# Kernel tuning notes

Hardware: AMD Instinct MI355X
Metric: run time of the kernel (lower is better)

## Reference

```python
import jax, jax.numpy as jnp
import numpy as np

HID = 128
NLAYERS = 8
LAT = 32
DIM_IN = 63 + 15 + LAT  # pe(xyz,L=10)=3+60, pe(shift,L=2)=3+12, latent=32 -> 110


def _pe(x, L):
    # NeRF positional encoding, include_input=True, freq-major [sin3,cos3] per freq
    freqs = (2.0 ** jnp.arange(L)).astype(x.dtype)
    xf = x[..., None, :] * freqs[:, None]                      # [..., L, 3]
    sc = jnp.concatenate([jnp.sin(xf), jnp.cos(xf)], axis=-1)  # [..., L, 6]
    return jnp.concatenate([x, sc.reshape(*x.shape[:-1], 6 * L)], axis=-1)


def setup_inputs() -> dict:
    key = jax.random.key(0)
    ks = jax.random.split(key, 24)
    B, P, V = 2, 32768, 5023
    d = {}
    d["pts"] = jax.random.normal(ks[0], (B, P, 3), jnp.float32)
    d["deformed_mesh_pts"] = jax.random.normal(ks[1], (B, V, 3), jnp.float32)
    d["cano_verts"] = jax.random.normal(ks[2], (1, V, 3), jnp.float32)
    d["motion_latent"] = jax.random.normal(ks[3], (B, P, LAT), jnp.float32)
    for i in range(NLAYERS):
        fin = DIM_IN if i == 0 else (DIM_IN + HID if i == NLAYERS // 2 else HID)
        d[f"w{i}"] = jax.random.normal(ks[4 + i], (HID, fin), jnp.float32) / np.sqrt(fin).astype(np.float32)
        d[f"b{i}"] = jnp.zeros((HID,), jnp.float32)
    d["w_out"] = jax.random.normal(ks[20], (3, HID), jnp.float32) * 0.01
    d["b_out"] = jnp.zeros((3,), jnp.float32)
    return d


def reference(pts, deformed_mesh_pts, cano_verts, motion_latent,
              w0, b0, w1, b1, w2, b2, w3, b3, w4, b4, w5, b5, w6, b6, w7, b7,
              w_out, b_out):
    # mesh-guided shift per vertex
    mesh_shift = cano_verts - deformed_mesh_pts                 # [B,V,3]
    # point-to-point NN search (squared euclidean cdist + argmin)
    d2 = ((pts ** 2).sum(-1)[:, :, None]
          + (deformed_mesh_pts ** 2).sum(-1)[:, None, :]
          - 2.0 * jnp.einsum('bpc,bvc->bpv', pts, deformed_mesh_pts))  # [B,P,V]
    d2 = jnp.maximum(d2, 0.0)
    idx = jnp.argmin(d2, axis=-1)                               # [B,P]
    dist = jnp.min(d2, axis=-1)                                 # [B,P]
    weight = jnp.exp(-dist)[..., None]                          # 1/exp(dist)
    gidx = jnp.broadcast_to(idx[:, :, None], idx.shape + (3,))
    gshift = jnp.take_along_axis(mesh_shift, gidx, axis=1) * weight  # [B,P,3]
    # deformation MLP with skip connection at layer 4
    initial = jnp.concatenate([_pe(pts, 10), _pe(gshift, 2), motion_latent], axis=-1)
    ws = [w0, w1, w2, w3, w4, w5, w6, w7]
    bs = [b0, b1, b2, b3, b4, b5, b6, b7]
    x = initial
    last_feat = x
    for i in range(NLAYERS):
        inp = jnp.concatenate([initial, x], axis=-1) if i == NLAYERS // 2 else x
        x = inp @ ws[i].T + bs[i]
        last_feat = x  # pre-activation feature (out_feat_ls[-1])
        x = jax.nn.relu(x)
    mlp_shift = x @ w_out.T + b_out                             # [B,P,3]
    pts_shifts = gshift + mlp_shift
    return pts + pts_shifts, last_feat
```

## Files before the change

kernel.cpp:

```cpp
#include <hip/hip_runtime.h>
#include <math.h>

typedef unsigned short ushort_t;
typedef unsigned int   uint_t;
typedef __attribute__((ext_vector_type(8)))  short bf16x8;
typedef __attribute__((ext_vector_type(16))) float f32x16;

#define NPTS   65536
#define NV     5023
#define LATD   32
#define KF     110
#define FSTR   112

__device__ __forceinline__ ushort_t f2bf(float f) {
  union { float f; unsigned u; } x; x.f = f;
  unsigned r = x.u + 0x7fffu + ((x.u >> 16) & 1u);
  return (ushort_t)(r >> 16);
}
__device__ __forceinline__ float bf2f(ushort_t u) {
  union { unsigned u; float f; } x; x.u = ((unsigned)u) << 16;
  return x.f;
}
__device__ __forceinline__ uint_t packsplit(float v) {
  const ushort_t h = f2bf(v);
  const ushort_t l = f2bf(v - bf2f(h));
  return (uint_t)h | ((uint_t)l << 16);
}


__global__ __launch_bounds__(256, 4) void k_nnfeat(
    const float* __restrict__ pts, const float* __restrict__ dm,
    const float* __restrict__ cano, const float* __restrict__ lat,
    const float* __restrict__ w0, const float* __restrict__ w1,
    const float* __restrict__ w2, const float* __restrict__ w3,
    const float* __restrict__ w4, const float* __restrict__ w5,
    const float* __restrict__ w6, const float* __restrict__ w7,
    uint_t* __restrict__ feat, float* __restrict__ base3,
    ushort_t* __restrict__ wsWh, ushort_t* __restrict__ wsWl)
{
  const int tid = threadIdx.x;

  if (tid < 144) {
    const int e = blockIdx.x * 144 + tid;
    const int p = e >> 14, local = e & 16383;
    const int j   = local & 7;
    const int lh  = (local >> 3) & 1;
    const int l31 = (local >> 4) & 31;
    const int tn  = (local >> 9) & 3;
    const int ks  = (local >> 11) & 7;
    const int n = tn*32 + l31;
    const int k = ks*16 + lh*8 + j;
    float v;
    if (p == 0)      v = (k < KF) ? w0[n*110 + k] : 0.f;
    else if (p == 1) v = w1[n*128 + k];
    else if (p == 2) v = w2[n*128 + k];
    else if (p == 3) v = w3[n*128 + k];
    else if (p == 4) v = (k < KF) ? w4[n*238 + k] : 0.f;
    else if (p == 5) v = w4[n*238 + KF + k];
    else if (p == 6) v = w5[n*128 + k];
    else if (p == 7) v = w6[n*128 + k];
    else             v = w7[n*128 + k];
    const ushort_t h = f2bf(v);
    wsWh[e] = h;
    wsWl[e] = f2bf(v - bf2f(h));
  }

  __shared__ float4 sV[512];
  __shared__ float  sD[64];
  __shared__ int    sI[64];

  const int lane = tid & 63, w = tid >> 6;
  const int slot = lane >> 4, s = lane & 15;
  const int g0 = blockIdx.x * 64;
  const int b  = blockIdx.x >> 9;
  const float* __restrict__ dmb = dm + b * NV * 3;
  const int pbase = g0 + w*16 + slot*4;

  float px[4], py[4], pz[4], p2[4], bs[4]; int bi[4];
  #pragma unroll
  for (int j = 0; j < 4; ++j) {
    px[j] = pts[(pbase+j)*3+0]; py[j] = pts[(pbase+j)*3+1]; pz[j] = pts[(pbase+j)*3+2];
    p2[j] = fmaf(px[j],px[j], fmaf(py[j],py[j], pz[j]*pz[j]));
    bs[j] = 3.4e38f; bi[j] = 0;
  }

  for (int v0 = 0; v0 < NV; v0 += 512) {
    __syncthreads();
    #pragma unroll
    for (int it = 0; it < 2; ++it) {
      const int i = it*256 + tid;
      const int v = v0 + i;
      float4 t;
      if (v < NV) {
        const float x = dmb[v*3+0], y = dmb[v*3+1], z = dmb[v*3+2];
        t = make_float4(x, y, z, fmaf(x,x, fmaf(y,y, z*z)));
      } else {
        t = make_float4(0.f, 0.f, 0.f, __builtin_inff());
      }
      sV[i] = t;
    }
    __syncthreads();
    #pragma unroll 8
    for (int k = 0; k < 32; ++k) {
      const float4 t = sV[k*16 + s];
      const int vi = v0 + k*16 + s;
      #pragma unroll
      for (int j = 0; j < 4; ++j) {
        const float dot = fmaf(px[j], t.x, fmaf(py[j], t.y, pz[j]*t.z));
        float d2 = fmaf(-2.f, dot, p2[j] + t.w);
        d2 = fmaxf(d2, 0.f);
        if (d2 < bs[j]) { bs[j] = d2; bi[j] = vi; }
      }
    }
  }

  #pragma unroll
  for (int off = 1; off <= 8; off <<= 1) {
    #pragma unroll
    for (int j = 0; j < 4; ++j) {
      const float ob = __shfl_xor(bs[j], off, 64);
      const int   oi = __shfl_xor(bi[j], off, 64);
      const bool take = (ob < bs[j]) || ((ob == bs[j]) && (oi < bi[j]));
      if (take) { bs[j] = ob; bi[j] = oi; }
    }
  }
  if (s == 0) {
    #pragma unroll
    for (int j = 0; j < 4; ++j) {
      sD[w*16 + slot*4 + j] = bs[j];
      sI[w*16 + slot*4 + j] = bi[j];
    }
  }
  __syncthreads();

  const int p = tid & 63, slice = tid >> 6;
  const int g = g0 + p;
  const float wd = sD[p];
  const int   wi = sI[p];

  const float qx = pts[g*3+0], qy = pts[g*3+1], qz = pts[g*3+2];
  const float wgt = expf(-wd);
  const float sx = (cano[wi*3+0] - dmb[wi*3+0]) * wgt;
  const float sy = (cano[wi*3+1] - dmb[wi*3+1]) * wgt;
  const float sz = (cano[wi*3+2] - dmb[wi*3+2]) * wgt;

  uint_t* __restrict__ fr = feat + (size_t)g * FSTR;

  if (slice == 0) {
    base3[g*3+0] = qx + sx; base3[g*3+1] = qy + sy; base3[g*3+2] = qz + sz;
    fr[0] = packsplit(qx); fr[1] = packsplit(qy); fr[2] = packsplit(qz);
    #pragma unroll
    for (int f = 0; f < 3; ++f) {
      const float F = (float)(1 << f);
      float s0,c0,s1,c1,s2,c2;
      sincosf(qx*F,&s0,&c0); sincosf(qy*F,&s1,&c1); sincosf(qz*F,&s2,&c2);
      const int k = 3 + 6*f;
      fr[k+0]=packsplit(s0); fr[k+1]=packsplit(s1); fr[k+2]=packsplit(s2);
      fr[k+3]=packsplit(c0); fr[k+4]=packsplit(c1); fr[k+5]=packsplit(c2);
    }
    fr[110] = 0; fr[111] = 0;
  } else if (slice == 1) {
    #pragma unroll
    for (int f = 3; f < 7; ++f) {
      const float F = (float)(1 << f);
      float s0,c0,s1,c1,s2,c2;
      sincosf(qx*F,&s0,&c0); sincosf(qy*F,&s1,&c1); sincosf(qz*F,&s2,&c2);
      const int k = 3 + 6*f;
      fr[k+0]=packsplit(s0); fr[k+1]=packsplit(s1); fr[k+2]=packsplit(s2);
      fr[k+3]=packsplit(c0); fr[k+4]=packsplit(c1); fr[k+5]=packsplit(c2);
    }
  } else if (slice == 2) {
    #pragma unroll
    for (int f = 7; f < 10; ++f) {
      const float F = (float)(1 << f);
      float s0,c0,s1,c1,s2,c2;
      sincosf(qx*F,&s0,&c0); sincosf(qy*F,&s1,&c1); sincosf(qz*F,&s2,&c2);
      const int k = 3 + 6*f;
      fr[k+0]=packsplit(s0); fr[k+1]=packsplit(s1); fr[k+2]=packsplit(s2);
      fr[k+3]=packsplit(c0); fr[k+4]=packsplit(c1); fr[k+5]=packsplit(c2);
    }
    #pragma unroll
    for (int j = 0; j < 16; ++j) fr[78+j] = packsplit(lat[g*LATD + j]);
  } else {
    fr[63]=packsplit(sx); fr[64]=packsplit(sy); fr[65]=packsplit(sz);
    #pragma unroll
    for (int f = 0; f < 2; ++f) {
      const float F = (float)(1 << f);
      float s0,c0,s1,c1,s2,c2;
      sincosf(sx*F,&s0,&c0); sincosf(sy*F,&s1,&c1); sincosf(sz*F,&s2,&c2);
      const int k = 66 + 6*f;
      fr[k+0]=packsplit(s0); fr[k+1]=packsplit(s1); fr[k+2]=packsplit(s2);
      fr[k+3]=packsplit(c0); fr[k+4]=packsplit(c1); fr[k+5]=packsplit(c2);
    }
    #pragma unroll
    for (int j = 16; j < 32; ++j) fr[78+j] = packsplit(lat[g*LATD + j]);
  }
}


union U4 { uint_t u[4]; bf16x8 v; };

__device__ __forceinline__ void zero4(f32x16 (&a)[4]) {
  #pragma unroll
  for (int i = 0; i < 4; ++i) a[i] = (f32x16)(0.f);
}

__device__ __forceinline__ void load_feat_frags(
    const uint_t* __restrict__ fr, bf16x8 (&Xh)[8], bf16x8 (&Xl)[8], int lh)
{
  #pragma unroll
  for (int ks = 0; ks < 7; ++ks) {
    const int k0 = ks*16 + lh*8;
    const uint4 ua = *(const uint4*)(fr + k0);
    const uint4 ub = *(const uint4*)(fr + k0 + 4);
    U4 H, L;
    H.u[0] = (ua.x & 0xffffu) | (ua.y << 16);
    H.u[1] = (ua.z & 0xffffu) | (ua.w << 16);
    H.u[2] = (ub.x & 0xffffu) | (ub.y << 16);
    H.u[3] = (ub.z & 0xffffu) | (ub.w << 16);
    L.u[0] = (ua.x >> 16) | (ua.y & 0xffff0000u);
    L.u[1] = (ua.z >> 16) | (ua.w & 0xffff0000u);
    L.u[2] = (ub.x >> 16) | (ub.y & 0xffff0000u);
    L.u[3] = (ub.z >> 16) | (ub.w & 0xffff0000u);
    Xh[ks] = H.v; Xl[ks] = L.v;
  }
}

__device__ __forceinline__ void load_slab(bf16x8 (&wh)[4], bf16x8 (&wl)[4],
    const ushort_t* __restrict__ Wh, const ushort_t* __restrict__ Wl,
    int ks, int l31, int lh)
{
  const int lo = l31*16 + lh*8;
  #pragma unroll
  for (int tn = 0; tn < 4; ++tn) {
    const int off = (ks*4 + tn)*512 + lo;
    wh[tn] = *(const bf16x8*)(Wh + off);
    wl[tn] = *(const bf16x8*)(Wl + off);
  }
}

__device__ __forceinline__ void mfma_slab(f32x16 (&acc)[4],
    const bf16x8 (&wh)[4], const bf16x8 (&wl)[4],
    const bf16x8& xh, const bf16x8& xl)
{
  #pragma unroll
  for (int tn = 0; tn < 4; ++tn) {
    acc[tn] = __builtin_amdgcn_mfma_f32_32x32x16_bf16(wh[tn], xh, acc[tn], 0,0,0);
    acc[tn] = __builtin_amdgcn_mfma_f32_32x32x16_bf16(wl[tn], xh, acc[tn], 0,0,0);
    acc[tn] = __builtin_amdgcn_mfma_f32_32x32x16_bf16(wh[tn], xl, acc[tn], 0,0,0);
  }
}

template<int NKS, bool TAIL>
__device__ __forceinline__ void run_panel(f32x16 (&acc)[4],
    const ushort_t* __restrict__ Wh, const ushort_t* __restrict__ Wl,
    const ushort_t* __restrict__ WhN, const ushort_t* __restrict__ WlN,
    bf16x8 (&wbh)[2][4], bf16x8 (&wbl)[2][4],
    const bf16x8 (&Xh)[8], const bf16x8 (&Xl)[8], int l31, int lh)
{
  #pragma unroll
  for (int ks = 0; ks < NKS; ++ks) {
    const int b = ks & 1;
    mfma_slab(acc, wbh[b], wbl[b], Xh[ks], Xl[ks]);
    if (ks + 2 < NKS) {
      load_slab(wbh[b], wbl[b], Wh, Wl, ks + 2, l31, lh);
    } else if (TAIL) {
      load_slab(wbh[b], wbl[b], WhN, WlN, ks & 1, l31, lh);
    }
  }
}

__device__ __forceinline__ void bias_relu(f32x16 (&acc)[4],
    const float* __restrict__ bias, int lh)
{
  #pragma unroll
  for (int tn = 0; tn < 4; ++tn)
    #pragma unroll
    for (int b = 0; b < 4; ++b) {
      const float4 b4 = *(const float4*)(bias + tn*32 + 8*b + 4*lh);
      acc[tn][4*b+0] = fmaxf(acc[tn][4*b+0] + b4.x, 0.f);
      acc[tn][4*b+1] = fmaxf(acc[tn][4*b+1] + b4.y, 0.f);
      acc[tn][4*b+2] = fmaxf(acc[tn][4*b+2] + b4.z, 0.f);
      acc[tn][4*b+3] = fmaxf(acc[tn][4*b+3] + b4.w, 0.f);
// ... 119 lines not shown
  build_frags(acc, Xh, Xl, lh);

  zero4(acc);
  run_panel<8,false>(acc, wsWh + 8*16384, wsWl + 8*16384,
                          (const ushort_t*)0, (const ushort_t*)0, wbh, wbl, Xh, Xl, l31, lh);

  float* __restrict__ sFw = &sF[wid][0];
  #pragma unroll
  for (int tn = 0; tn < 4; ++tn)
    #pragma unroll
    for (int b = 0; b < 4; ++b) {
      const int n0 = tn*32 + 8*b + 4*lh;
      const float4 bv = *(const float4*)(sB + 7*128 + n0);
      const float v0 = acc[tn][4*b+0] + bv.x;
      const float v1 = acc[tn][4*b+1] + bv.y;
      const float v2 = acc[tn][4*b+2] + bv.z;
      const float v3 = acc[tn][4*b+3] + bv.w;
      *(float4*)(sFw + l31*132 + n0) = make_float4(v0, v1, v2, v3);
      acc[tn][4*b+0] = fmaxf(v0, 0.f);
      acc[tn][4*b+1] = fmaxf(v1, 0.f);
      acc[tn][4*b+2] = fmaxf(v2, 0.f);
      acc[tn][4*b+3] = fmaxf(v3, 0.f);
    }

  asm volatile("s_waitcnt lgkmcnt(0)" ::: "memory");
  __builtin_amdgcn_sched_barrier(0);

  float* __restrict__ out1 = out + (size_t)NPTS * 3;
  #pragma unroll
  for (int i = 0; i < 16; ++i) {
    const int idx = i*64 + lane;
    const int p = idx >> 5, q = idx & 31;
    const float4 v = *(const float4*)(sFw + p*132 + q*4);
    *(float4*)(out1 + (size_t)(p0 + p)*128 + q*4) = v;
  }

  float dotc[3];
  #pragma unroll
  for (int c = 0; c < 3; ++c) {
    float a = 0.f;
    #pragma unroll
    for (int tn = 0; tn < 4; ++tn)
      #pragma unroll
      for (int b = 0; b < 4; ++b) {
        const int n0 = tn*32 + 8*b + 4*lh;
        const float4 w4 = *(const float4*)(sB + 1024 + c*128 + n0);
        a = fmaf(acc[tn][4*b+0], w4.x, a);
        a = fmaf(acc[tn][4*b+1], w4.y, a);
        a = fmaf(acc[tn][4*b+2], w4.z, a);
        a = fmaf(acc[tn][4*b+3], w4.w, a);
      }
    a += __shfl_xor(a, 32, 64);
    dotc[c] = a;
  }
  if (lh == 0) {
    const int g = p0 + l31;
    #pragma unroll
    for (int c = 0; c < 3; ++c)
      out[g*3 + c] = base3[g*3 + c] + dotc[c] + sB[1408 + c];
  }
}

extern "C" void kernel_launch(void* const* d_in, const int* in_sizes, int n_in,
                              void* d_out, int out_size, void* d_ws, size_t ws_size,
                              hipStream_t stream)
{
  const float* pts  = (const float*)d_in[0];
  const float* dm   = (const float*)d_in[1];
  const float* cano = (const float*)d_in[2];
  const float* lat  = (const float*)d_in[3];
  const float* w[8]; const float* b[8];
  for (int i = 0; i < 8; ++i) {
    w[i] = (const float*)d_in[4 + 2*i];
    b[i] = (const float*)d_in[5 + 2*i];
  }
  const float* w_out = (const float*)d_in[20];
  const float* b_out = (const float*)d_in[21];
  float* out = (float*)d_out;

  uint_t*   feat  = (uint_t*)d_ws;
  float*    base3 = (float*)((char*)d_ws + (size_t)NPTS*FSTR*4);
  ushort_t* wsWh  = (ushort_t*)((char*)base3 + (size_t)NPTS*3*4);
  ushort_t* wsWl  = wsWh + 147456;

  k_nnfeat<<<1024, 256, 0, stream>>>(pts, dm, cano, lat,
      w[0],w[1],w[2],w[3],w[4],w[5],w[6],w[7], feat, base3, wsWh, wsWl);
  k_mlp<<<NPTS/128, 256, 0, stream>>>(feat, base3, wsWh, wsWl,
      b[0],b[1],b[2],b[3],b[4],b[5],b[6],b[7], w_out, b_out, out);
}
```

Measured before the change: 252.2 us.

## Split NN search into packed-FMA group minima pass with exact rescan of candidate groups

Adds a prep kernel that converts the weights to bf16 hi/lo and precomputes vertex pairs as (-2x,-2y,-2z,|v|^2) in pair-interleaved form. The NN kernel then gives each wave a quarter of the vertices and one point per lane. A first pass computes per-group minima with two-wide packed FMAs; a second pass rescans, with the original exact distance formula, only the groups whose minimum is within a small margin of the global minimum. This removes the per-vertex compare/select and LDS staging from most of the search, but adds an extra launch, a vpre buffer and reliance on the fixed margin for correct argmin.

```diff
diff --git a/kernel.cpp b/kernel.cpp
--- a/kernel.cpp
+++ b/kernel.cpp
@@ -5,12 +5,15 @@
 typedef unsigned int   uint_t;
 typedef __attribute__((ext_vector_type(8)))  short bf16x8;
 typedef __attribute__((ext_vector_type(16))) float f32x16;
+typedef __attribute__((ext_vector_type(2)))  float f32x2;
 
 #define NPTS   65536
 #define NV     5023
 #define LATD   32
 #define KF     110
 #define FSTR   112
+#define NPAIR  2512
+#define QPAIR  628
 
 __device__ __forceinline__ ushort_t f2bf(float f) {
   union { float f; unsigned u; } x; x.f = f;
@@ -27,21 +30,17 @@
   return (uint_t)h | ((uint_t)l << 16);
 }
 
-
-__global__ __launch_bounds__(256, 4) void k_nnfeat(
-    const float* __restrict__ pts, const float* __restrict__ dm,
-    const float* __restrict__ cano, const float* __restrict__ lat,
+__global__ __launch_bounds__(256) void k_prep(
+    const float* __restrict__ dm,
     const float* __restrict__ w0, const float* __restrict__ w1,
     const float* __restrict__ w2, const float* __restrict__ w3,
     const float* __restrict__ w4, const float* __restrict__ w5,
     const float* __restrict__ w6, const float* __restrict__ w7,
-    uint_t* __restrict__ feat, float* __restrict__ base3,
-    ushort_t* __restrict__ wsWh, ushort_t* __restrict__ wsWl)
-{
-  const int tid = threadIdx.x;
-
-  if (tid < 144) {
-    const int e = blockIdx.x * 144 + tid;
+    ushort_t* __restrict__ wsWh, ushort_t* __restrict__ wsWl,
+    float* __restrict__ vpre)
+{
+  const int e = blockIdx.x * 256 + threadIdx.x;
+  {
     const int p = e >> 14, local = e & 16383;
     const int j   = local & 7;
     const int lh  = (local >> 3) & 1;
@@ -64,79 +63,130 @@
     wsWh[e] = h;
     wsWl[e] = f2bf(v - bf2f(h));
   }
-
-  __shared__ float4 sV[512];
-  __shared__ float  sD[64];
-  __shared__ int    sI[64];
-
-  const int lane = tid & 63, w = tid >> 6;
-  const int slot = lane >> 4, s = lane & 15;
-  const int g0 = blockIdx.x * 64;
-  const int b  = blockIdx.x >> 9;
-  const float* __restrict__ dmb = dm + b * NV * 3;
-  const int pbase = g0 + w*16 + slot*4;
-
-  float px[4], py[4], pz[4], p2[4], bs[4]; int bi[4];
-  #pragma unroll
-  for (int j = 0; j < 4; ++j) {
-    px[j] = pts[(pbase+j)*3+0]; py[j] = pts[(pbase+j)*3+1]; pz[j] = pts[(pbase+j)*3+2];
-    p2[j] = fmaf(px[j],px[j], fmaf(py[j],py[j], pz[j]*pz[j]));
-    bs[j] = 3.4e38f; bi[j] = 0;
-  }
-
-  for (int v0 = 0; v0 < NV; v0 += 512) {
-    __syncthreads();
-    #pragma unroll
-    for (int it = 0; it < 2; ++it) {
-      const int i = it*256 + tid;
-      const int v = v0 + i;
-      float4 t;
-      if (v < NV) {
-        const float x = dmb[v*3+0], y = dmb[v*3+1], z = dmb[v*3+2];
-        t = make_float4(x, y, z, fmaf(x,x, fmaf(y,y, z*z)));
-      } else {
-        t = make_float4(0.f, 0.f, 0.f, __builtin_inff());
+  if (e < 2*NPAIR) {
+    const int b  = (e >= NPAIR) ? 1 : 0;
+    const int pr = e - b*NPAIR;
+    const float* __restrict__ dmb = dm + b*NV*3;
+    const int v0 = 2*pr, v1 = v0 + 1;
+    const float x0 = dmb[v0*3+0], y0 = dmb[v0*3+1], z0 = dmb[v0*3+2];
+    const float w0v = fmaf(x0,x0, fmaf(y0,y0, z0*z0));
+    float x1, y1, z1, w1v;
+    if (v1 < NV) {
+      x1 = dmb[v1*3+0]; y1 = dmb[v1*3+1]; z1 = dmb[v1*3+2];
+      w1v = fmaf(x1,x1, fmaf(y1,y1, z1*z1));
+    } else { x1 = 0.f; y1 = 0.f; z1 = 0.f; w1v = 3.0e38f; }
+    float* __restrict__ q = vpre + (size_t)e * 8;
+    q[0] = -2.f*x0; q[1] = -2.f*x1;
+    q[2] = -2.f*y0; q[3] = -2.f*y1;
+    q[4] = -2.f*z0; q[5] = -2.f*z1;
+    q[6] = w0v;     q[7] = w1v;
+  }
+}
+
+#define MARGIN 2.0e-3f
+
+__global__ __launch_bounds__(256, 4) void k_nnfeat(
+    const float* __restrict__ pts, const float* __restrict__ dm,
+    const float* __restrict__ cano, const float* __restrict__ lat,
+    const float* __restrict__ vpre,
+    uint_t* __restrict__ feat, float* __restrict__ base3)
+{
+  __shared__ float sMin[256];
+  __shared__ float sDr[256];
+  __shared__ int   sIr[256];
+
+  const int tid = threadIdx.x;
+  const int l   = tid & 63;
+  const int wid = tid >> 6;
+  const int g0  = blockIdx.x * 64;
+  const int b   = blockIdx.x >> 9;
+  const int gpt = g0 + l;
+
+  const float px = pts[gpt*3+0], py = pts[gpt*3+1], pz = pts[gpt*3+2];
+  const float p2 = fmaf(px,px, fmaf(py,py, pz*pz));
+
+  const int wu = __builtin_amdgcn_readfirstlane(wid);
+  const float* __restrict__ vp = vpre + ((size_t)b*NPAIR + (size_t)wu*QPAIR) * 8;
+
+  const f32x2 px2 = {px,px}, py2 = {py,py}, pz2 = {pz,pz};
+
+  f32x2 gm[16];
+  #pragma unroll
+  for (int g = 0; g < 16; ++g) {
+    f32x2 m = {3.0e38f, 3.0e38f};
+    const int cnt = (g == 15) ? (QPAIR - 15*40) : 40;
+    const float* __restrict__ q = vp + g*40*8;
+    #pragma unroll 4
+    for (int t = 0; t < cnt; ++t) {
+      const f32x2 vx = *(const f32x2*)(q + t*8 + 0);
+      const f32x2 vy = *(const f32x2*)(q + t*8 + 2);
+      const f32x2 vz = *(const f32x2*)(q + t*8 + 4);
+      const f32x2 vw = *(const f32x2*)(q + t*8 + 6);
+      f32x2 s = __builtin_elementwise_fma(vx, px2, vw);
+      s = __builtin_elementwise_fma(vy, py2, s);
+      s = __builtin_elementwise_fma(vz, pz2, s);
+      m = __builtin_elementwise_min(m, s);
+    }
+    gm[g] = m;
+  }
+
+  f32x2 mm = gm[0];
+  #pragma unroll
+  for (int g = 1; g < 16; ++g) mm = __builtin_elementwise_min(mm, gm[g]);
+  sMin[wid*64 + l] = fminf(mm.x, mm.y);
+  __syncthreads();
+  const float thr = fminf(fminf(sMin[l], sMin[64 + l]),
+                          fminf(sMin[128 + l], sMin[192 + l])) + MARGIN;
+
+  float bs = 3.4e38f; int bi = 0;
+  uint_t hm = 0;
+  #pragma unroll
+  for (int g = 0; g < 16; ++g)
+    if (fminf(gm[g].x, gm[g].y) <= thr) hm |= (1u << g);
+  const int vbase = wu * (2*QPAIR);
+  while (hm != 0) {
+    const int g = __ffs(hm) - 1; hm &= hm - 1;
+    const int base = g*40;
+    #pragma unroll 4
+    for (int t = 0; t < 40; ++t) {
+      const int pr = base + t;
+      if (pr < QPAIR) {
+        const float* q = vp + (size_t)pr*8;
+        const float4 qa = *(const float4*)q;
+        const float4 qb = *(const float4*)(q + 4);
+        const float x0 = qa.x*-0.5f, x1 = qa.y*-0.5f;
+        const float y0 = qa.z*-0.5f, y1 = qa.w*-0.5f;
+        const float z0 = qb.x*-0.5f, z1 = qb.y*-0.5f;
+        const float w0 = qb.z,       w1 = qb.w;
+        const int vi0 = vbase + 2*pr;
+        {
+          const float dot = fmaf(px, x0, fmaf(py, y0, pz*z0));
+          float d2 = fmaf(-2.f, dot, p2 + w0);
+          d2 = fmaxf(d2, 0.f);
+          if (d2 < bs) { bs = d2; bi = vi0; }
+        }
+        {
+          const float dot = fmaf(px, x1, fmaf(py, y1, pz*z1));
+          float d2 = fmaf(-2.f, dot, p2 + w1);
+          d2 = fmaxf(d2, 0.f);
+          if (d2 < bs) { bs = d2; bi = vi0 + 1; }
+        }
       }
-      sV[i] = t;
-    }
-    __syncthreads();
-    #pragma unroll 8
-    for (int k = 0; k < 32; ++k) {
-      const float4 t = sV[k*16 + s];
-      const int vi = v0 + k*16 + s;
-      #pragma unroll
-      for (int j = 0; j < 4; ++j) {
-        const float dot = fmaf(px[j], t.x, fmaf(py[j], t.y, pz[j]*t.z));
-        float d2 = fmaf(-2.f, dot, p2[j] + t.w);
-        d2 = fmaxf(d2, 0.f);
-        if (d2 < bs[j]) { bs[j] = d2; bi[j] = vi; }
-      }
-    }
-  }
-
-  #pragma unroll
-  for (int off = 1; off <= 8; off <<= 1) {
-    #pragma unroll
-    for (int j = 0; j < 4; ++j) {
-      const float ob = __shfl_xor(bs[j], off, 64);
-      const int   oi = __shfl_xor(bi[j], off, 64);
-      const bool take = (ob < bs[j]) || ((ob == bs[j]) && (oi < bi[j]));
-      if (take) { bs[j] = ob; bi[j] = oi; }
-    }
-  }
-  if (s == 0) {
-    #pragma unroll
-    for (int j = 0; j < 4; ++j) {
-      sD[w*16 + slot*4 + j] = bs[j];
-      sI[w*16 + slot*4 + j] = bi[j];
-    }
-  }
+    }
+  }
+  sDr[wid*64 + l] = bs;
+  sIr[wid*64 + l] = bi;
   __syncthreads();
 
   const int p = tid & 63, slice = tid >> 6;
   const int g = g0 + p;
-  const float wd = sD[p];
-  const int   wi = sI[p];
+  float wd = sDr[p]; int wi = sIr[p];
+  #pragma unroll
+  for (int w_ = 1; w_ < 4; ++w_) {
+    const float od = sDr[w_*64 + p]; const int oi = sIr[w_*64 + p];
+    if (od < wd || (od == wd && oi < wi)) { wd = od; wi = oi; }
+  }
+  const float* __restrict__ dmb = dm + b * NV * 3;
 
   const float qx = pts[g*3+0], qy = pts[g*3+1], qz = pts[g*3+2];
   const float wgt = expf(-wd);
@@ -484,9 +534,11 @@
   float*    base3 = (float*)((char*)d_ws + (size_t)NPTS*FSTR*4);
   ushort_t* wsWh  = (ushort_t*)((char*)base3 + (size_t)NPTS*3*4);
   ushort_t* wsWl  = wsWh + 147456;
-
-  k_nnfeat<<<1024, 256, 0, stream>>>(pts, dm, cano, lat,
-      w[0],w[1],w[2],w[3],w[4],w[5],w[6],w[7], feat, base3, wsWh, wsWl);
+  float*    vpre  = (float*)(wsWl + 147456);
+
+  k_prep<<<576, 256, 0, stream>>>(dm,
+      w[0],w[1],w[2],w[3],w[4],w[5],w[6],w[7], wsWh, wsWl, vpre);
+  k_nnfeat<<<1024, 256, 0, stream>>>(pts, dm, cano, lat, vpre, feat, base3);
   k_mlp<<<NPTS/128, 256, 0, stream>>>(feat, base3, wsWh, wsWl,
       b[0],b[1],b[2],b[3],b[4],b[5],b[6],b[7], w_out, b_out, out);
 }
```

Result: no change. 255.9 us (+1.5%).

## Two-pass NN search with packed-FMA min pruning and sincos double-angle recurrence

Applied to the files above, without the earlier changes.

Moves vertex preprocessing (SoA pairs with precomputed squared norms) and weight splitting into a separate prep kernel. The NN search becomes two passes. The first computes per-chunk minimum distances with packed two-wide FMAs and min ops, skipping argmin bookkeeping. The second rescans only the chunks whose minimum lies within a small margin of the global minimum, computing exact distances and indices. Positional-encoding sincos calls are replaced by double-angle recurrences, which adds rounding drift at higher frequencies and a margin-dependent risk of picking a different neighbour.

```diff
diff --git a/kernel.cpp b/kernel.cpp
--- a/kernel.cpp
+++ b/kernel.cpp
@@ -5,12 +5,16 @@
 typedef unsigned int   uint_t;
 typedef __attribute__((ext_vector_type(8)))  short bf16x8;
 typedef __attribute__((ext_vector_type(16))) float f32x16;
+typedef __attribute__((ext_vector_type(2)))  float f32x2;
 
 #define NPTS   65536
 #define NV     5023
+#define NVP    5120
+#define NPRB   2560
 #define LATD   32
 #define KF     110
 #define FSTR   112
+#define MARGIN 2.0e-3f
 
 __device__ __forceinline__ ushort_t f2bf(float f) {
   union { float f; unsigned u; } x; x.f = f;
@@ -27,21 +31,24 @@
   return (uint_t)h | ((uint_t)l << 16);
 }
 
-
-__global__ __launch_bounds__(256, 4) void k_nnfeat(
-    const float* __restrict__ pts, const float* __restrict__ dm,
-    const float* __restrict__ cano, const float* __restrict__ lat,
+__device__ __forceinline__ void dbl_step(float& s, float& c) {
+  const float t = s * c;
+  const float cn = fmaf(-2.f * s, s, 1.f);
+  s = t + t;
+  c = cn;
+}
+
+__global__ __launch_bounds__(256) void k_prep(
+    const float* __restrict__ dm,
     const float* __restrict__ w0, const float* __restrict__ w1,
     const float* __restrict__ w2, const float* __restrict__ w3,
     const float* __restrict__ w4, const float* __restrict__ w5,
     const float* __restrict__ w6, const float* __restrict__ w7,
-    uint_t* __restrict__ feat, float* __restrict__ base3,
-    ushort_t* __restrict__ wsWh, ushort_t* __restrict__ wsWl)
-{
-  const int tid = threadIdx.x;
-
-  if (tid < 144) {
-    const int e = blockIdx.x * 144 + tid;
+    ushort_t* __restrict__ wsWh, ushort_t* __restrict__ wsWl,
+    float4* __restrict__ vpreA, float4* __restrict__ vpreB)
+{
+  const int e = blockIdx.x * 256 + threadIdx.x;
+  {
     const int p = e >> 14, local = e & 16383;
     const int j   = local & 7;
     const int lh  = (local >> 3) & 1;
@@ -64,52 +71,145 @@
     wsWh[e] = h;
     wsWl[e] = f2bf(v - bf2f(h));
   }
-
-  __shared__ float4 sV[512];
-  __shared__ float  sD[64];
-  __shared__ int    sI[64];
-
+  if (e < 2*NPRB) {
+    const int b  = (e >= NPRB) ? 1 : 0;
+    const int pr = e - b*NPRB;
+    const float* __restrict__ dmb = dm + b*NV*3;
+    const int v0 = 2*pr, v1 = v0 + 1;
+    float x0=0.f, y0=0.f, z0=0.f, w0v=3.0e38f;
+    float x1=0.f, y1=0.f, z1=0.f, w1v=3.0e38f;
+    if (v0 < NV) {
+      x0 = dmb[v0*3+0]; y0 = dmb[v0*3+1]; z0 = dmb[v0*3+2];
+      w0v = fmaf(x0,x0, fmaf(y0,y0, z0*z0));
+    }
+    if (v1 < NV) {
+      x1 = dmb[v1*3+0]; y1 = dmb[v1*3+1]; z1 = dmb[v1*3+2];
+      w1v = fmaf(x1,x1, fmaf(y1,y1, z1*z1));
+    }
+    vpreA[b*NPRB + pr] = make_float4(x0, x1, y0, y1);
+    vpreB[b*NPRB + pr] = make_float4(z0, z1, w0v, w1v);
+  }
+}
+
+__global__ __launch_bounds__(256, 4) void k_nnfeat(
+    const float* __restrict__ pts, const float* __restrict__ dm,
+    const float* __restrict__ cano, const float* __restrict__ lat,
+    const float4* __restrict__ vpreA, const float4* __restrict__ vpreB,
+    uint_t* __restrict__ feat, float* __restrict__ base3)
+{
+  __shared__ __align__(16) float4 sVa[256];
+  __shared__ __align__(16) float4 sVb[256];
+  __shared__ float sD[64];
+  __shared__ int   sI[64];
+
+  const int tid = threadIdx.x;
   const int lane = tid & 63, w = tid >> 6;
   const int slot = lane >> 4, s = lane & 15;
   const int g0 = blockIdx.x * 64;
   const int b  = blockIdx.x >> 9;
-  const float* __restrict__ dmb = dm + b * NV * 3;
   const int pbase = g0 + w*16 + slot*4;
 
-  float px[4], py[4], pz[4], p2[4], bs[4]; int bi[4];
+  const float4* __restrict__ vA = vpreA + b*NPRB;
+  const float4* __restrict__ vB = vpreB + b*NPRB;
+
+  f32x2 MX[4], MY[4], MZ[4];
+  float p2[4];
   #pragma unroll
   for (int j = 0; j < 4; ++j) {
-    px[j] = pts[(pbase+j)*3+0]; py[j] = pts[(pbase+j)*3+1]; pz[j] = pts[(pbase+j)*3+2];
-    p2[j] = fmaf(px[j],px[j], fmaf(py[j],py[j], pz[j]*pz[j]));
-    bs[j] = 3.4e38f; bi[j] = 0;
-  }
-
-  for (int v0 = 0; v0 < NV; v0 += 512) {
-    __syncthreads();
-    #pragma unroll
-    for (int it = 0; it < 2; ++it) {
-      const int i = it*256 + tid;
-      const int v = v0 + i;
-      float4 t;
-      if (v < NV) {
-        const float x = dmb[v*3+0], y = dmb[v*3+1], z = dmb[v*3+2];
-        t = make_float4(x, y, z, fmaf(x,x, fmaf(y,y, z*z)));
-      } else {
-        t = make_float4(0.f, 0.f, 0.f, __builtin_inff());
+    const float px = pts[(pbase+j)*3+0], py = pts[(pbase+j)*3+1], pz = pts[(pbase+j)*3+2];
+    p2[j] = fmaf(px,px, fmaf(py,py, pz*pz));
+    MX[j] = (f32x2){-2.f*px, -2.f*px};
+    MY[j] = (f32x2){-2.f*py, -2.f*py};
+    MZ[j] = (f32x2){-2.f*pz, -2.f*pz};
+  }
+
+  float gm[5][4];
+  #pragma unroll
+  for (int sc = 0; sc < 5; ++sc) {
+    f32x2 m0 = {3.0e38f, 3.0e38f}, m1 = m0, m2 = m0, m3 = m0;
+    #pragma unroll
+    for (int h = 0; h < 2; ++h) {
+      const int c = sc*2 + h;
+      __syncthreads();
+      sVa[tid] = vA[c*256 + tid];
+      sVb[tid] = vB[c*256 + tid];
+      __syncthreads();
+      #pragma unroll 8
+      for (int kk = 0; kk < 16; ++kk) {
+        const int pr = kk*16 + s;
+        const float4 qa = sVa[pr];
+        const float4 qb = sVb[pr];
+        const f32x2 xx = {qa.x, qa.y}, yy = {qa.z, qa.w};
+        const f32x2 zz = {qb.x, qb.y}, ww = {qb.z, qb.w};
+        f32x2 t;
+        t = __builtin_elementwise_fma(xx, MX[0], ww);
+        t = __builtin_elementwise_fma(yy, MY[0], t);
+        t = __builtin_elementwise_fma(zz, MZ[0], t);
+        m0 = __builtin_elementwise_min(m0, t);
+        t = __builtin_elementwise_fma(xx, MX[1], ww);
+        t = __builtin_elementwise_fma(yy, MY[1], t);
+        t = __builtin_elementwise_fma(zz, MZ[1], t);
+        m1 = __builtin_elementwise_min(m1, t);
+        t = __builtin_elementwise_fma(xx, MX[2], ww);
+        t = __builtin_elementwise_fma(yy, MY[2], t);
+        t = __builtin_elementwise_fma(zz, MZ[2], t);
+        m2 = __builtin_elementwise_min(m2, t);
+        t = __builtin_elementwise_fma(xx, MX[3], ww);
+        t = __builtin_elementwise_fma(yy, MY[3], t);
+        t = __builtin_elementwise_fma(zz, MZ[3], t);
+        m3 = __builtin_elementwise_min(m3, t);
       }
-      sV[i] = t;
-    }
-    __syncthreads();
-    #pragma unroll 8
-    for (int k = 0; k < 32; ++k) {
-      const float4 t = sV[k*16 + s];
-      const int vi = v0 + k*16 + s;
+    }
+    gm[sc][0] = fminf(m0.x, m0.y);
+    gm[sc][1] = fminf(m1.x, m1.y);
+    gm[sc][2] = fminf(m2.x, m2.y);
+    gm[sc][3] = fminf(m3.x, m3.y);
+  }
+
+  float thr[4];
+  #pragma unroll
+  for (int j = 0; j < 4; ++j) {
+    float mv = gm[0][j];
+    #pragma unroll
+    for (int sc = 1; sc < 5; ++sc) mv = fminf(mv, gm[sc][j]);
+    #pragma unroll
+    for (int off = 1; off <= 8; off <<= 1)
+      mv = fminf(mv, __shfl_xor(mv, off, 64));
+    thr[j] = mv + MARGIN;
+  }
+
+  float bs[4]; int bi[4];
+  #pragma unroll
+  for (int j = 0; j < 4; ++j) { bs[j] = 3.4e38f; bi[j] = 0; }
+  uint_t hm = 0;
+  #pragma unroll
+  for (int sc = 0; sc < 5; ++sc)
+    if (gm[sc][0] <= thr[0] || gm[sc][1] <= thr[1] ||
+        gm[sc][2] <= thr[2] || gm[sc][3] <= thr[3]) hm |= (1u << sc);
+  while (hm) {
+    const int sc = __ffs(hm) - 1; hm &= hm - 1;
+    const int prb = sc*512;
+    #pragma unroll 4
+    for (int kk = 0; kk < 32; ++kk) {
+      const int pr = prb + kk*16 + s;
+      const float4 qa = vA[pr];
+      const float4 qb = vB[pr];
+      const int vi0 = 2*pr;
       #pragma unroll
       for (int j = 0; j < 4; ++j) {
-        const float dot = fmaf(px[j], t.x, fmaf(py[j], t.y, pz[j]*t.z));
-        float d2 = fmaf(-2.f, dot, p2[j] + t.w);
-        d2 = fmaxf(d2, 0.f);
-        if (d2 < bs[j]) { bs[j] = d2; bi[j] = vi; }
+        const float px = -0.5f*MX[j].x, py = -0.5f*MY[j].x, pz = -0.5f*MZ[j].x;
+        {
+          const float dot = fmaf(px, qa.x, fmaf(py, qa.z, pz*qb.x));
+          float d2 = fmaf(-2.f, dot, p2[j] + qb.z);
+          d2 = fmaxf(d2, 0.f);
+          if (d2 < bs[j]) { bs[j] = d2; bi[j] = vi0; }
+        }
+        {
+          const float dot = fmaf(px, qa.y, fmaf(py, qa.w, pz*qb.y));
+          float d2 = fmaf(-2.f, dot, p2[j] + qb.w);
+          d2 = fmaxf(d2, 0.f);
+          if (d2 < bs[j]) { bs[j] = d2; bi[j] = vi0 + 1; }
+        }
       }
     }
   }
@@ -137,6 +237,7 @@
   const int g = g0 + p;
   const float wd = sD[p];
   const int   wi = sI[p];
+  const float* __restrict__ dmb = dm + b * NV * 3;
 
   const float qx = pts[g*3+0], qy = pts[g*3+1], qz = pts[g*3+2];
   const float wgt = expf(-wd);
@@ -149,48 +250,48 @@
   if (slice == 0) {
     base3[g*3+0] = qx + sx; base3[g*3+1] = qy + sy; base3[g*3+2] = qz + sz;
     fr[0] = packsplit(qx); fr[1] = packsplit(qy); fr[2] = packsplit(qz);
+    float s0,c0,s1,c1,s2,c2;
+    sincosf(qx,&s0,&c0); sincosf(qy,&s1,&c1); sincosf(qz,&s2,&c2);
     #pragma unroll
     for (int f = 0; f < 3; ++f) {
-      const float F = (float)(1 << f);
-      float s0,c0,s1,c1,s2,c2;
-      sincosf(qx*F,&s0,&c0); sincosf(qy*F,&s1,&c1); sincosf(qz*F,&s2,&c2);
       const int k = 3 + 6*f;
       fr[k+0]=packsplit(s0); fr[k+1]=packsplit(s1); fr[k+2]=packsplit(s2);
       fr[k+3]=packsplit(c0); fr[k+4]=packsplit(c1); fr[k+5]=packsplit(c2);
+      if (f < 2) { dbl_step(s0,c0); dbl_step(s1,c1); dbl_step(s2,c2); }
     }
     fr[110] = 0; fr[111] = 0;
   } else if (slice == 1) {
+    float s0,c0,s1,c1,s2,c2;
+    sincosf(qx*8.f,&s0,&c0); sincosf(qy*8.f,&s1,&c1); sincosf(qz*8.f,&s2,&c2);
     #pragma unroll
     for (int f = 3; f < 7; ++f) {
-      const float F = (float)(1 << f);
-      float s0,c0,s1,c1,s2,c2;
-      sincosf(qx*F,&s0,&c0); sincosf(qy*F,&s1,&c1); sincosf(qz*F,&s2,&c2);
       const int k = 3 + 6*f;
       fr[k+0]=packsplit(s0); fr[k+1]=packsplit(s1); fr[k+2]=packsplit(s2);
       fr[k+3]=packsplit(c0); fr[k+4]=packsplit(c1); fr[k+5]=packsplit(c2);
+      if (f < 6) { dbl_step(s0,c0); dbl_step(s1,c1); dbl_step(s2,c2); }
     }
   } else if (slice == 2) {
+    float s0,c0,s1,c1,s2,c2;
+    sincosf(qx*128.f,&s0,&c0); sincosf(qy*128.f,&s1,&c1); sincosf(qz*128.f,&s2,&c2);
     #pragma unroll
     for (int f = 7; f < 10; ++f) {
-      const float F = (float)(1 << f);
-      float s0,c0,s1,c1,s2,c2;
-      sincosf(qx*F,&s0,&c0); sincosf(qy*F,&s1,&c1); sincosf(qz*F,&s2,&c2);
       const int k = 3 + 6*f;
       fr[k+0]=packsplit(s0); fr[k+1]=packsplit(s1); fr[k+2]=packsplit(s2);
       fr[k+3]=packsplit(c0); fr[k+4]=packsplit(c1); fr[k+5]=packsplit(c2);
+      if (f < 9) { dbl_step(s0,c0); dbl_step(s1,c1); dbl_step(s2,c2); }
     }
     #pragma unroll
     for (int j = 0; j < 16; ++j) fr[78+j] = packsplit(lat[g*LATD + j]);
   } else {
     fr[63]=packsplit(sx); fr[64]=packsplit(sy); fr[65]=packsplit(sz);
+    float s0,c0,s1,c1,s2,c2;
+    sincosf(sx,&s0,&c0); sincosf(sy,&s1,&c1); sincosf(sz,&s2,&c2);
     #pragma unroll
     for (int f = 0; f < 2; ++f) {
-      const float F = (float)(1 << f);
-      float s0,c0,s1,c1,s2,c2;
-      sincosf(sx*F,&s0,&c0); sincosf(sy*F,&s1,&c1); sincosf(sz*F,&s2,&c2);
       const int k = 66 + 6*f;
       fr[k+0]=packsplit(s0); fr[k+1]=packsplit(s1); fr[k+2]=packsplit(s2);
       fr[k+3]=packsplit(c0); fr[k+4]=packsplit(c1); fr[k+5]=packsplit(c2);
+      if (f < 1) { dbl_step(s0,c0); dbl_step(s1,c1); dbl_step(s2,c2); }
     }
     #pragma unroll
     for (int j = 16; j < 32; ++j) fr[78+j] = packsplit(lat[g*LATD + j]);
@@ -484,9 +585,12 @@
   float*    base3 = (float*)((char*)d_ws + (size_t)NPTS*FSTR*4);
   ushort_t* wsWh  = (ushort_t*)((char*)base3 + (size_t)NPTS*3*4);
   ushort_t* wsWl  = wsWh + 147456;
-
-  k_nnfeat<<<1024, 256, 0, stream>>>(pts, dm, cano, lat,
-      w[0],w[1],w[2],w[3],w[4],w[5],w[6],w[7], feat, base3, wsWh, wsWl);
+  float4*   vpreA = (float4*)(wsWl + 147456);
+  float4*   vpreB = vpreA + 2*NPRB;
+
+  k_prep<<<576, 256, 0, stream>>>(dm,
+      w[0],w[1],w[2],w[3],w[4],w[5],w[6],w[7], wsWh, wsWl, vpreA, vpreB);
+  k_nnfeat<<<1024, 256, 0, stream>>>(pts, dm, cano, lat, vpreA, vpreB, feat, base3);
   k_mlp<<<NPTS/128, 256, 0, stream>>>(feat, base3, wsWh, wsWl,
       b[0],b[1],b[2],b[3],b[4],b[5],b[6],b[7], w_out, b_out, out);
 }
```

New measurement: 258.4 us. +2.5%, slower.

## Compute NN distances with MFMA split-bf16 prefilter and exact fp32 rescoring

Applied to the files above, without the earlier changes.

Moves the brute-force nearest-vertex search onto MFMA. A new prep kernel packs the vertices into split-bf16 fragments, and one matrix multiply yields approximate squared distances for 32 points by 32 vertices at a time. A first pass finds the approximate minimum, and a second pass recomputes exact fp32 distances only for vertices within a fixed margin of it. Positional-encoding sin/cos are now built by the angle-doubling recurrence instead of one sincos per frequency. This trades scalar ALU work for two MFMA sweeps, with risks from the fixed margin and from error accumulating through the doubling steps.

```diff
diff --git a/kernel.cpp b/kernel.cpp
--- a/kernel.cpp
+++ b/kernel.cpp
@@ -8,9 +8,14 @@
 
 #define NPTS   65536
 #define NV     5023
+#define NVP    5120
+#define NTILE  160
 #define LATD   32
 #define KF     110
 #define FSTR   112
+#define MARGIN 1.5e-2f
+
+union U4 { uint_t u[4]; bf16x8 v; };
 
 __device__ __forceinline__ ushort_t f2bf(float f) {
   union { float f; unsigned u; } x; x.f = f;
@@ -27,21 +32,25 @@
   return (uint_t)h | ((uint_t)l << 16);
 }
 
-
-__global__ __launch_bounds__(256, 4) void k_nnfeat(
-    const float* __restrict__ pts, const float* __restrict__ dm,
-    const float* __restrict__ cano, const float* __restrict__ lat,
+__device__ __forceinline__ void dbl_step(float& s, float& c) {
+  const float t = s * c;
+  const float cn = fmaf(-2.f * s, s, 1.f);
+  s = t + t;
+  c = cn;
+}
+
+__global__ __launch_bounds__(256) void k_prep(
+    const float* __restrict__ dm,
     const float* __restrict__ w0, const float* __restrict__ w1,
     const float* __restrict__ w2, const float* __restrict__ w3,
     const float* __restrict__ w4, const float* __restrict__ w5,
     const float* __restrict__ w6, const float* __restrict__ w7,
-    uint_t* __restrict__ feat, float* __restrict__ base3,
-    ushort_t* __restrict__ wsWh, ushort_t* __restrict__ wsWl)
-{
-  const int tid = threadIdx.x;
-
-  if (tid < 144) {
-    const int e = blockIdx.x * 144 + tid;
+    ushort_t* __restrict__ wsWh, ushort_t* __restrict__ wsWl,
+    ushort_t* __restrict__ aFF, ushort_t* __restrict__ aFH,
+    float4* __restrict__ vq)
+{
+  const int e = blockIdx.x * 256 + threadIdx.x;
+  {
     const int p = e >> 14, local = e & 16383;
     const int j   = local & 7;
     const int lh  = (local >> 3) & 1;
@@ -64,79 +73,128 @@
     wsWh[e] = h;
     wsWl[e] = f2bf(v - bf2f(h));
   }
-
-  __shared__ float4 sV[512];
-  __shared__ float  sD[64];
-  __shared__ int    sI[64];
-
+  if (e < 2*NVP) {
+    const int b = (e >= NVP) ? 1 : 0;
+    const int v = e - b*NVP;
+    const float* __restrict__ dmb = dm + b*NV*3;
+    float x = 0.f, y = 0.f, z = 0.f, wv = 3.0e38f;
+    if (v < NV) {
+      x = dmb[v*3+0]; y = dmb[v*3+1]; z = dmb[v*3+2];
+      wv = fmaf(x,x, fmaf(y,y, z*z));
+    }
+    const ushort_t hx = f2bf(x),  hy = f2bf(y),  hz = f2bf(z),  hw = f2bf(wv);
+    const ushort_t lx = f2bf(x - bf2f(hx)), ly = f2bf(y - bf2f(hy));
+    const ushort_t lz = f2bf(z - bf2f(hz)), lw = f2bf(wv - bf2f(hw));
+    U4 F, H;
+    F.u[0] = (uint_t)hx | ((uint_t)hy << 16);
+    F.u[1] = (uint_t)hz | ((uint_t)hw << 16);
+    F.u[2] = (uint_t)lx | ((uint_t)ly << 16);
+    F.u[3] = (uint_t)lz | ((uint_t)lw << 16);
+    H.u[0] = F.u[0]; H.u[1] = F.u[1]; H.u[2] = 0; H.u[3] = 0;
+    *(bf16x8*)(aFF + (size_t)e*8) = F.v;
+    *(bf16x8*)(aFH + (size_t)e*8) = H.v;
+    vq[e] = make_float4(x, y, z, wv);
+  }
+}
+
+__global__ __launch_bounds__(256, 2) void k_nnfeat(
+    const float* __restrict__ pts, const float* __restrict__ dm,
+    const float* __restrict__ cano, const float* __restrict__ lat,
+    const ushort_t* __restrict__ aFF, const ushort_t* __restrict__ aFH,
+    const float4* __restrict__ vq,
+    uint_t* __restrict__ feat, float* __restrict__ base3)
+{
+  __shared__ float sD[128];
+  __shared__ int   sI[128];
+
+  const int tid = threadIdx.x;
   const int lane = tid & 63, w = tid >> 6;
-  const int slot = lane >> 4, s = lane & 15;
-  const int g0 = blockIdx.x * 64;
-  const int b  = blockIdx.x >> 9;
-  const float* __restrict__ dmb = dm + b * NV * 3;
-  const int pbase = g0 + w*16 + slot*4;
-
-  float px[4], py[4], pz[4], p2[4], bs[4]; int bi[4];
-  #pragma unroll
-  for (int j = 0; j < 4; ++j) {
-    px[j] = pts[(pbase+j)*3+0]; py[j] = pts[(pbase+j)*3+1]; pz[j] = pts[(pbase+j)*3+2];
-    p2[j] = fmaf(px[j],px[j], fmaf(py[j],py[j], pz[j]*pz[j]));
-    bs[j] = 3.4e38f; bi[j] = 0;
-  }
-
-  for (int v0 = 0; v0 < NV; v0 += 512) {
-    __syncthreads();
-    #pragma unroll
-    for (int it = 0; it < 2; ++it) {
-      const int i = it*256 + tid;
-      const int v = v0 + i;
-      float4 t;
-      if (v < NV) {
-        const float x = dmb[v*3+0], y = dmb[v*3+1], z = dmb[v*3+2];
-        t = make_float4(x, y, z, fmaf(x,x, fmaf(y,y, z*z)));
-      } else {
-        t = make_float4(0.f, 0.f, 0.f, __builtin_inff());
+  const int l31 = lane & 31, lh = lane >> 5;
+  const int g0 = blockIdx.x * 128;
+  const int b  = blockIdx.x >> 8;
+  const int pt = g0 + w*32 + l31;
+
+  const float px = pts[pt*3+0], py = pts[pt*3+1], pz = pts[pt*3+2];
+  const float p2 = fmaf(px,px, fmaf(py,py, pz*pz));
+
+  const float tpx = -2.f*px, tpy = -2.f*py, tpz = -2.f*pz;
+  const ushort_t hpx = f2bf(tpx), hpy = f2bf(tpy), hpz = f2bf(tpz);
+  const ushort_t lpx = f2bf(tpx - bf2f(hpx));
+  const ushort_t lpy = f2bf(tpy - bf2f(hpy));
+  const ushort_t lpz = f2bf(tpz - bf2f(hpz));
+  U4 Bh, Bl;
+  Bh.u[0] = (uint_t)hpx | ((uint_t)hpy << 16);
+  Bh.u[1] = (uint_t)hpz | (0x3F80u << 16);
+  Bh.u[2] = Bh.u[0]; Bh.u[3] = Bh.u[1];
+  Bl.u[0] = (uint_t)lpx | ((uint_t)lpy << 16);
+  Bl.u[1] = (uint_t)lpz;
+  Bl.u[2] = 0; Bl.u[3] = 0;
+  const bf16x8 bfrag = lh ? Bl.v : Bh.v;
+
+  const ushort_t* __restrict__ aBase = (lh ? aFH : aFF) + (size_t)b * NVP * 8;
+  const float4*   __restrict__ vqb   = vq + (size_t)b * NVP;
+
+  const f32x16 zacc = (f32x16)(0.f);
+
+  float gmin = 3.0e38f;
+  #pragma unroll 4
+  for (int t = 0; t < NTILE; ++t) {
+    const bf16x8 a = *(const bf16x8*)(aBase + (size_t)(t*32 + l31)*8);
+    const f32x16 d = __builtin_amdgcn_mfma_f32_32x32x16_bf16(a, bfrag, zacc, 0,0,0);
+    const float t0 = fminf(fminf(d[0],d[1]),   fminf(d[2],d[3]));
+    const float t1 = fminf(fminf(d[4],d[5]),   fminf(d[6],d[7]));
+    const float t2 = fminf(fminf(d[8],d[9]),   fminf(d[10],d[11]));
+    const float t3 = fminf(fminf(d[12],d[13]), fminf(d[14],d[15]));
+    gmin = fminf(gmin, fminf(fminf(t0,t1), fminf(t2,t3)));
+  }
+  gmin = fminf(gmin, __shfl_xor(gmin, 32, 64));
+  const float thr = gmin + MARGIN;
+
+  float bs = 3.4e38f; int bi = 0;
+  #pragma unroll 2
+  for (int t = 0; t < NTILE; ++t) {
+    const bf16x8 a = *(const bf16x8*)(aBase + (size_t)(t*32 + l31)*8);
+    const f32x16 d = __builtin_amdgcn_mfma_f32_32x32x16_bf16(a, bfrag, zacc, 0,0,0);
+    float q4[4];
+    q4[0] = fminf(fminf(d[0],d[1]),   fminf(d[2],d[3]));
+    q4[1] = fminf(fminf(d[4],d[5]),   fminf(d[6],d[7]));
+    q4[2] = fminf(fminf(d[8],d[9]),   fminf(d[10],d[11]));
+    q4[3] = fminf(fminf(d[12],d[13]), fminf(d[14],d[15]));
+    const float tm = fminf(fminf(q4[0],q4[1]), fminf(q4[2],q4[3]));
+    if (tm <= thr) {
+      #pragma unroll
+      for (int q = 0; q < 4; ++q) {
+        if (q4[q] <= thr) {
+          #pragma unroll
+          for (int rr = 0; rr < 4; ++rr) {
+            const int r = q*4 + rr;
+            if (d[r] <= thr) {
+              const int row = (r & 3) + 8*(r >> 2) + 4*lh;
+              const int v = t*32 + row;
+              const float4 qv = vqb[v];
+              const float dot = fmaf(px, qv.x, fmaf(py, qv.y, pz*qv.z));
+              float d2 = fmaf(-2.f, dot, p2 + qv.w);
+              d2 = fmaxf(d2, 0.f);
+              if (d2 < bs || (d2 == bs && v < bi)) { bs = d2; bi = v; }
+            }
+          }
+        }
       }
-      sV[i] = t;
-    }
-    __syncthreads();
-    #pragma unroll 8
-    for (int k = 0; k < 32; ++k) {
-      const float4 t = sV[k*16 + s];
-      const int vi = v0 + k*16 + s;
-      #pragma unroll
-      for (int j = 0; j < 4; ++j) {
-        const float dot = fmaf(px[j], t.x, fmaf(py[j], t.y, pz[j]*t.z));
-        float d2 = fmaf(-2.f, dot, p2[j] + t.w);
-        d2 = fmaxf(d2, 0.f);
-        if (d2 < bs[j]) { bs[j] = d2; bi[j] = vi; }
-      }
-    }
-  }
-
-  #pragma unroll
-  for (int off = 1; off <= 8; off <<= 1) {
-    #pragma unroll
-    for (int j = 0; j < 4; ++j) {
-      const float ob = __shfl_xor(bs[j], off, 64);
-      const int   oi = __shfl_xor(bi[j], off, 64);
-      const bool take = (ob < bs[j]) || ((ob == bs[j]) && (oi < bi[j]));
-      if (take) { bs[j] = ob; bi[j] = oi; }
-    }
-  }
-  if (s == 0) {
-    #pragma unroll
-    for (int j = 0; j < 4; ++j) {
-      sD[w*16 + slot*4 + j] = bs[j];
-      sI[w*16 + slot*4 + j] = bi[j];
-    }
-  }
+    }
+  }
+  {
+    const float ob = __shfl_xor(bs, 32, 64);
+    const int   oi = __shfl_xor(bi, 32, 64);
+    if (ob < bs || (ob == bs && oi < bi)) { bs = ob; bi = oi; }
+  }
+  if (lh == 0) { sD[w*32 + l31] = bs; sI[w*32 + l31] = bi; }
   __syncthreads();
 
-  const int p = tid & 63, slice = tid >> 6;
+  const int p = tid & 127, slice = tid >> 7;
   const int g = g0 + p;
   const float wd = sD[p];
   const int   wi = sI[p];
+  const float* __restrict__ dmb = dm + b * NV * 3;
 
   const float qx = pts[g*3+0], qy = pts[g*3+1], qz = pts[g*3+2];
   const float wgt = expf(-wd);
@@ -149,56 +207,48 @@
   if (slice == 0) {
     base3[g*3+0] = qx + sx; base3[g*3+1] = qy + sy; base3[g*3+2] = qz + sz;
     fr[0] = packsplit(qx); fr[1] = packsplit(qy); fr[2] = packsplit(qz);
+    float s0,c0,s1,c1,s2,c2;
+    sincosf(qx,&s0,&c0); sincosf(qy,&s1,&c1); sincosf(qz,&s2,&c2);
     #pragma unroll
     for (int f = 0; f < 3; ++f) {
-      const float F = (float)(1 << f);
-      float s0,c0,s1,c1,s2,c2;
-      sincosf(qx*F,&s0,&c0); sincosf(qy*F,&s1,&c1); sincosf(qz*F,&s2,&c2);
       const int k = 3 + 6*f;
       fr[k+0]=packsplit(s0); fr[k+1]=packsplit(s1); fr[k+2]=packsplit(s2);
       fr[k+3]=packsplit(c0); fr[k+4]=packsplit(c1); fr[k+5]=packsplit(c2);
-    }
-    fr[110] = 0; fr[111] = 0;
-  } else if (slice == 1) {
+      if (f < 2) { dbl_step(s0,c0); dbl_step(s1,c1); dbl_step(s2,c2); }
+    }
+    sincosf(qx*8.f,&s0,&c0); sincosf(qy*8.f,&s1,&c1); sincosf(qz*8.f,&s2,&c2);
     #pragma unroll
     for (int f = 3; f < 7; ++f) {
-      const float F = (float)(1 << f);
-      float s0,c0,s1,c1,s2,c2;
-      sincosf(qx*F,&s0,&c0); sincosf(qy*F,&s1,&c1); sincosf(qz*F,&s2,&c2);
       const int k = 3 + 6*f;
       fr[k+0]=packsplit(s0); fr[k+1]=packsplit(s1); fr[k+2]=packsplit(s2);
       fr[k+3]=packsplit(c0); fr[k+4]=packsplit(c1); fr[k+5]=packsplit(c2);
-    }
-  } else if (slice == 2) {
+      if (f < 6) { dbl_step(s0,c0); dbl_step(s1,c1); dbl_step(s2,c2); }
+    }
+  } else {
+    float s0,c0,s1,c1,s2,c2;
+    sincosf(qx*128.f,&s0,&c0); sincosf(qy*128.f,&s1,&c1); sincosf(qz*128.f,&s2,&c2);
     #pragma unroll
     for (int f = 7; f < 10; ++f) {
-      const float F = (float)(1 << f);
-      float s0,c0,s1,c1,s2,c2;
-      sincosf(qx*F,&s0,&c0); sincosf(qy*F,&s1,&c1); sincosf(qz*F,&s2,&c2);
       const int k = 3 + 6*f;
       fr[k+0]=packsplit(s0); fr[k+1]=packsplit(s1); fr[k+2]=packsplit(s2);
       fr[k+3]=packsplit(c0); fr[k+4]=packsplit(c1); fr[k+5]=packsplit(c2);
-    }
-    #pragma unroll
-    for (int j = 0; j < 16; ++j) fr[78+j] = packsplit(lat[g*LATD + j]);
-  } else {
+      if (f < 9) { dbl_step(s0,c0); dbl_step(s1,c1); dbl_step(s2,c2); }
+    }
     fr[63]=packsplit(sx); fr[64]=packsplit(sy); fr[65]=packsplit(sz);
+    sincosf(sx,&s0,&c0); sincosf(sy,&s1,&c1); sincosf(sz,&s2,&c2);
     #pragma unroll
     for (int f = 0; f < 2; ++f) {
-      const float F = (float)(1 << f);
-      float s0,c0,s1,c1,s2,c2;
-      sincosf(sx*F,&s0,&c0); sincosf(sy*F,&s1,&c1); sincosf(sz*F,&s2,&c2);
       const int k = 66 + 6*f;
       fr[k+0]=packsplit(s0); fr[k+1]=packsplit(s1); fr[k+2]=packsplit(s2);
       fr[k+3]=packsplit(c0); fr[k+4]=packsplit(c1); fr[k+5]=packsplit(c2);
-    }
-    #pragma unroll
-    for (int j = 16; j < 32; ++j) fr[78+j] = packsplit(lat[g*LATD + j]);
-  }
-}
-
-
-union U4 { uint_t u[4]; bf16x8 v; };
+      if (f < 1) { dbl_step(s0,c0); dbl_step(s1,c1); dbl_step(s2,c2); }
+    }
+    #pragma unroll
+    for (int j = 0; j < 32; ++j) fr[78+j] = packsplit(lat[g*LATD + j]);
+    fr[110] = 0; fr[111] = 0;
+  }
+}
+
 
 __device__ __forceinline__ void zero4(f32x16 (&a)[4]) {
   #pragma unroll
@@ -484,9 +534,13 @@
   float*    base3 = (float*)((char*)d_ws + (size_t)NPTS*FSTR*4);
   ushort_t* wsWh  = (ushort_t*)((char*)base3 + (size_t)NPTS*3*4);
   ushort_t* wsWl  = wsWh + 147456;
-
-  k_nnfeat<<<1024, 256, 0, stream>>>(pts, dm, cano, lat,
-      w[0],w[1],w[2],w[3],w[4],w[5],w[6],w[7], feat, base3, wsWh, wsWl);
+  ushort_t* aFF   = wsWl + 147456;
+  ushort_t* aFH   = aFF + 2*NVP*8;
+  float4*   vq    = (float4*)(aFH + 2*NVP*8);
+
+  k_prep<<<576, 256, 0, stream>>>(dm,
+      w[0],w[1],w[2],w[3],w[4],w[5],w[6],w[7], wsWh, wsWl, aFF, aFH, vq);
+  k_nnfeat<<<512, 256, 0, stream>>>(pts, dm, cano, lat, aFF, aFH, vq, feat, base3);
   k_mlp<<<NPTS/128, 256, 0, stream>>>(feat, base3, wsWh, wsWl,
       b[0],b[1],b[2],b[3],b[4],b[5],b[6],b[7], w_out, b_out, out);
 }
```

Result: slower. 261.2 us (+3.6%).
